# Kernel optimization log

Hardware: AMD Instinct MI355X
Metric: run time of the kernel (lower is better)

Reference implementation:

```python
import jax, jax.numpy as jnp
import numpy as np

EPS = 1e-6

def _linear_params(key, d_in, d_out):
    w = jax.random.normal(key, (d_in, d_out), dtype=jnp.float32) * np.sqrt(2.0 / (d_in + d_out))
    b = jnp.zeros((d_out,), dtype=jnp.float32)
    return w, b

def setup_inputs() -> dict:
    key = jax.random.key(0)
    ks = jax.random.split(key, 8)
    B, S, D = 4, 2048, 1024
    x = jax.random.normal(ks[0], (B, S, D), dtype=jnp.float32)
    wq, bq = _linear_params(ks[1], D, D)
    wk, bk = _linear_params(ks[2], D, D)
    wv, bv = _linear_params(ks[3], D, D)
    wo, bo = _linear_params(ks[4], D, D)
    w1, b1 = _linear_params(ks[5], D, D)
    w2, b2 = _linear_params(ks[6], D, D)
    g1 = jnp.ones((D,), jnp.float32); be1 = jnp.zeros((D,), jnp.float32)
    g2 = jnp.ones((D,), jnp.float32); be2 = jnp.zeros((D,), jnp.float32)
    return {"x": x, "wq": wq, "bq": bq, "wk": wk, "bk": bk, "wv": wv, "bv": bv,
            "wo": wo, "bo": bo, "w1": w1, "b1": b1, "w2": w2, "b2": b2,
            "g1": g1, "be1": be1, "g2": g2, "be2": be2}

def _layernorm(x, gamma, beta):
    mean = jnp.mean(x, axis=-1, keepdims=True)
    # torch .std() default is unbiased (ddof=1); eps added to std (not var)
    std = jnp.std(x, axis=-1, keepdims=True, ddof=1)
    return gamma * (x - mean) / (std + EPS) + beta

def _attention(x, wq, bq, wk, bk, wv, bv, wo, bo):
    S = x.shape[-2]
    q = x @ wq + bq  # [B,S,D]
    k = x @ wk + bk
    v = x @ wv + bv
    scores = jnp.einsum('bsd,btd->bst', q, k) / jnp.sqrt(jnp.asarray(S, jnp.float32))
    causal = jnp.tril(jnp.ones((S, S), dtype=bool))  # keep lower triangle incl. diag
    scores = jnp.where(causal, scores, -jnp.inf)
    attn = jax.nn.softmax(scores, axis=-1)
    out = jnp.einsum('bst,btd->bsd', attn, v)
    return out @ wo + bo

def reference(x, wq, bq, wk, bk, wv, bv, wo, bo, w1, b1, w2, b2, g1, be1, g2, be2):
    h = _attention(_layernorm(x, g1, be1), wq, bq, wk, bk, wv, bv, wo, bo) + x
    m = _layernorm(h, g2, be2)
    m = jnp.maximum(m @ w1 + b1, 0.0) @ w2 + b2
    return m + h
```

## Files before the change

### kernel.cpp

```cpp
#include <hip/hip_runtime.h>
#include <math.h>

#define BB 4
#define SS 2048
#define DD 1024
#define MM (BB*SS)
#define SD ((size_t)SS*DD)
#define MD ((size_t)MM*DD)
#define PPB ((size_t)2162688)

#define WT_OFF (3*MD + 4*PPB)
#define ZP_OFF (WT_OFF + 6*(size_t)DD*DD)
#define REQ_WS ((ZP_OFF + 16) * 2)

constexpr float LN_EPS = 1e-6f;

typedef __attribute__((ext_vector_type(8))) __bf16 bf16x8;
typedef __attribute__((ext_vector_type(4))) float f32x4;

__device__ __forceinline__ unsigned short f2bfbits(float f){
    unsigned u = __float_as_uint(f);
    u += 0x7FFFu + ((u >> 16) & 1u);
    return (unsigned short)(u >> 16);
}
__device__ __forceinline__ int rowWidth(int s){ return ((s >> 6) + 1) << 6; }
__device__ __forceinline__ size_t rowOff(int s){
    int g = s >> 6;
    return (size_t)4096 * (size_t)((g * (g + 1)) >> 1) + (size_t)(s & 63) * (size_t)((g + 1) << 6);
}
__device__ __forceinline__ void gl_lds(const unsigned short* g, unsigned short* l){
    __builtin_amdgcn_global_load_lds(
        (const __attribute__((address_space(1))) unsigned int*)g,
        (__attribute__((address_space(3))) unsigned int*)l, 16, 0, 0);
}

__device__ __forceinline__ int3 xcd_swz(){
    const int gx = gridDim.x, gy = gridDim.y, gz = gridDim.z;
    const int n = gx * gy * gz;
    int lin = blockIdx.x + gx * (blockIdx.y + gy * blockIdx.z);
    const int cpx = n >> 3;
    lin = (lin & 7) * cpx + (lin >> 3);
    int3 r;
    r.x = lin % gx; lin /= gx;
    r.y = lin % gy;
    r.z = lin / gy;
    return r;
}

__global__ __launch_bounds__(256)
void sentinel_kernel(float* __restrict__ out, const float val){
    out[(size_t)blockIdx.x * 256 + threadIdx.x] = val;
}

struct WPack { const float* w[6]; unsigned short* o[6]; unsigned short* zp; };
__global__ __launch_bounds__(256)
void wtrans(WPack wp)
{
    __shared__ float Ts[64][65];
    const float* W = wp.w[blockIdx.z];
    unsigned short* WT = wp.o[blockIdx.z];
    const int r0 = blockIdx.y*64, c0 = blockIdx.x*64;
    const int tid = threadIdx.x;
    if (blockIdx.x == 0 && blockIdx.y == 0 && blockIdx.z == 0 && tid < 16) wp.zp[tid] = 0;
    #pragma unroll
    for (int i = 0; i < 16; ++i){
        int lin = tid + i*256;
        int r = lin >> 6, c = lin & 63;
        Ts[r][c] = W[(size_t)(r0+r)*DD + c0+c];
    }
    __syncthreads();
    #pragma unroll
    for (int i = 0; i < 16; ++i){
        int lin = tid + i*256;
        int r = lin >> 6, c = lin & 63;
        WT[(size_t)(c0+r)*DD + r0+c] = f2bfbits(Ts[c][r]);
    }
}

__global__ __launch_bounds__(256)
void ln_f32(const float* __restrict__ x, const float* __restrict__ gamma,
            const float* __restrict__ beta, unsigned short* __restrict__ out)
{
    __shared__ float red[4];
    const int row = blockIdx.x;
    const int tid = threadIdx.x;
    float4 xv = ((const float4*)(x + (size_t)row*DD))[tid];
    float v[4] = {xv.x, xv.y, xv.z, xv.w};
    float s = v[0]+v[1]+v[2]+v[3];
    #pragma unroll
    for (int off = 32; off > 0; off >>= 1) s += __shfl_down(s, off, 64);
    if ((tid & 63) == 0) red[tid >> 6] = s;
    __syncthreads();
    const float mean = (red[0]+red[1]+red[2]+red[3]) * (1.0f/DD);
    __syncthreads();
    float q = 0.f;
    #pragma unroll
    for (int i = 0; i < 4; ++i){ float d = v[i]-mean; q += d*d; }
    #pragma unroll
    for (int off = 32; off > 0; off >>= 1) q += __shfl_down(q, off, 64);
    if ((tid & 63) == 0) red[tid >> 6] = q;
    __syncthreads();
    const float var = (red[0]+red[1]+red[2]+red[3]) * (1.0f/(DD-1));
    const float inv = 1.0f/(sqrtf(var) + LN_EPS);
    float4 g4 = ((const float4*)gamma)[tid];
    float4 b4 = ((const float4*)beta)[tid];
    ushort4 o;
    o.x = f2bfbits(g4.x*(v[0]-mean)*inv + b4.x);
    o.y = f2bfbits(g4.y*(v[1]-mean)*inv + b4.y);
    o.z = f2bfbits(g4.z*(v[2]-mean)*inv + b4.z);
    o.w = f2bfbits(g4.w*(v[3]-mean)*inv + b4.w);
    ((ushort4*)(out + (size_t)row*DD))[tid] = o;
}

template<bool RELU, bool RES, bool OUTF, bool BIAS_M>
__device__ __forceinline__ void gemm_core(
    const unsigned short* __restrict__ A, const unsigned short* __restrict__ B,
    const float* __restrict__ bias, const float* __restrict__ resF,
    unsigned short* __restrict__ outB, float* __restrict__ outF,
    const int N, const int K, const int lda, const int ldb,
    const int m0, const int n0,
    unsigned short* As, unsigned short* Bs)
{
    const int tid = threadIdx.x, lane = tid & 63, wave = tid >> 6;
    const int wm = ((wave >> 1) & 1) * 64, wn = (wave & 1) * 64;
    const int quad = lane >> 4, l15 = lane & 15;
    const unsigned short* ga[4]; const unsigned short* gb[4];
    #pragma unroll
    for (int c = 0; c < 4; ++c){
        const int mr = (wave*4 + c)*8 + (lane >> 3);
        const int gk = ((lane & 7) - mr) & 7;
        ga[c] = A + (size_t)(m0 + mr)*lda + gk*8;
        gb[c] = B + (size_t)(n0 + mr)*ldb + gk*8;
    }
    f32x4 acc[4][4] = {};
    for (int k0 = 0; k0 < K; k0 += 64){
        #pragma unroll
        for (int c = 0; c < 4; ++c){
            gl_lds(ga[c] + k0, &As[(wave*4+c)*512]);
            gl_lds(gb[c] + k0, &Bs[(wave*4+c)*512]);
        }
        __syncthreads();
        #pragma unroll
        for (int kk = 0; kk < 2; ++kk){
            bf16x8 af[4], bfr[4];
            #pragma unroll
            for (int t = 0; t < 4; ++t){
                const int ra = wm + t*16 + l15, rb = wn + t*16 + l15, gi = kk*4 + quad;
                af[t]  = *(const bf16x8*)&As[ra*64 + (((gi + ra) & 7) << 3)];
                bfr[t] = *(const bf16x8*)&Bs[rb*64 + (((gi + rb) & 7) << 3)];
            }
            #pragma unroll
            for (int i = 0; i < 4; ++i)
                #pragma unroll
                for (int j = 0; j < 4; ++j)
                    acc[i][j] = __builtin_amdgcn_mfma_f32_16x16x32_bf16(af[i], bfr[j], acc[i][j], 0, 0, 0);
        }
        __syncthreads();
    }
    #pragma unroll
    for (int i = 0; i < 4; ++i){
        #pragma unroll
        for (int r = 0; r < 4; ++r){
            const int m = m0 + wm + i*16 + quad*4 + r;
            const float bm = BIAS_M ? bias[m] : 0.f;
            #pragma unroll
            for (int j = 0; j < 4; ++j){
                const int n = n0 + wn + j*16 + l15;
                float v = acc[i][j][r] + (BIAS_M ? bm : bias[n]);
                if constexpr (RELU) v = fmaxf(v, 0.f);
                if constexpr (RES) v += resF[(size_t)m*N + n];
                if constexpr (OUTF) outF[(size_t)m*N + n] = v;
                else outB[(size_t)m*N + n] = f2bfbits(v);
            }
        }
    }
}

template<bool RELU, bool RES, bool OUTF, bool BIAS_M>
__global__ __launch_bounds__(256)
void gemm_mfma(const unsigned short* __restrict__ A, const unsigned short* __restrict__ B,
               const float* __restrict__ bias, const float* __restrict__ resF,
               unsigned short* __restrict__ outB, float* __restrict__ outF,
               const int N, const int K, const int lda, const int ldb)
{
    __shared__ unsigned short As[128*64];
    __shared__ unsigned short Bs[128*64];
    const int3 b = xcd_swz();
    gemm_core<RELU,RES,OUTF,BIAS_M>(A, B, bias, resF, outB, outF, N, K, lda, ldb,
                                    b.y*128, b.x*128, As, Bs);
}

__global__ __launch_bounds__(256)
void gemm_qk(const unsigned short* __restrict__ LN,
             const unsigned short* __restrict__ WqT, const unsigned short* __restrict__ WkT,
             const float* __restrict__ bq, const float* __restrict__ bk,
             unsigned short* __restrict__ Qw, unsigned short* __restrict__ Kw)
{
    __shared__ unsigned short As[128*64];
    __shared__ unsigned short Bs[128*64];
    const int3 b = xcd_swz();
    const bool isK = (b.z != 0);
    gemm_core<false,false,false,false>(LN, isK ? WkT : WqT, isK ? bk : bq, nullptr,
                                       isK ? Kw : Qw, nullptr, DD, DD, DD, DD,
                                       b.y*128, b.x*128, As, Bs);
}

__global__ __launch_bounds__(256)
void scores_mfma(const unsigned short* __restrict__ Qb, const unsigned short* __restrict__ Kb,
                 unsigned short* __restrict__ Pb, const float scale)
{
    const int3 b = xcd_swz();
    const int s0 = b.y*128, t0 = b.x*128;
    if (t0 > s0) return;
    const unsigned short* Q  = Qb + (size_t)b.z*SD;
    const unsigned short* Km = Kb + (size_t)b.z*SD;
    unsigned short* P        = Pb + (size_t)b.z*PPB;
    __shared__ unsigned short As[128*64];
    __shared__ unsigned short Bs[128*64];
    const int tid = threadIdx.x, lane = tid & 63, wave = tid >> 6;
    const int wm = ((wave >> 1) & 1) * 64, wn = (wave & 1) * 64;
    const int quad = lane >> 4, l15 = lane & 15;
    const unsigned short* ga[4]; const unsigned short* gb[4];
    #pragma unroll
    for (int c = 0; c < 4; ++c){
        const int mr = (wave*4 + c)*8 + (lane >> 3);
        const int gk = ((lane & 7) - mr) & 7;
        ga[c] = Q  + (size_t)(s0 + mr)*DD + gk*8;
        gb[c] = Km + (size_t)(t0 + mr)*DD + gk*8;
    }
    f32x4 acc[4][4] = {};
    for (int k0 = 0; k0 < DD; k0 += 64){
        #pragma unroll
        for (int c = 0; c < 4; ++c){
            gl_lds(ga[c] + k0, &As[(wave*4+c)*512]);
            gl_lds(gb[c] + k0, &Bs[(wave*4+c)*512]);
        }
        __syncthreads();
        #pragma unroll
        for (int kk = 0; kk < 2; ++kk){
            bf16x8 af[4], bfr[4];
            #pragma unroll
            for (int t = 0; t < 4; ++t){
                const int ra = wm + t*16 + l15, rb = wn + t*16 + l15, gi = kk*4 + quad;
                af[t]  = *(const bf16x8*)&As[ra*64 + (((gi + ra) & 7) << 3)];
                bfr[t] = *(const bf16x8*)&Bs[rb*64 + (((gi + rb) & 7) << 3)];
            }
            #pragma unroll
            for (int i = 0; i < 4; ++i)
                #pragma unroll
                for (int j = 0; j < 4; ++j)
                    acc[i][j] = __builtin_amdgcn_mfma_f32_16x16x32_bf16(af[i], bfr[j], acc[i][j], 0, 0, 0);
        }
        __syncthreads();
    }
    #pragma unroll
    for (int i = 0; i < 4; ++i){
        #pragma unroll
        for (int r = 0; r < 4; ++r){
            const int s = s0 + wm + i*16 + quad*4 + r;
            const int width = rowWidth(s);
            unsigned short* pr = P + rowOff(s);
            #pragma unroll
            for (int j = 0; j < 4; ++j){
                const int t = t0 + wn + j*16 + l15;
                if (t < width) pr[t] = f2bfbits(acc[i][j][r] * scale);
            }
        }
    }
}

__global__ __launch_bounds__(256)
void softmax_p(unsigned short* __restrict__ Pb)
{
    __shared__ float red[4];
    const int s = blockIdx.x;
    const int width = rowWidth(s);
    unsigned short* r = Pb + (size_t)blockIdx.y * PPB + rowOff(s);
    const int tid = threadIdx.x;
    float vals[8];
    float m = -1e30f;
    #pragma unroll
    for (int i = 0; i < 8; ++i){
        int t = tid + i*256;
        float v = -1e30f;
        if (t <= s) v = __uint_as_float(((unsigned)r[t]) << 16);
        vals[i] = v; m = fmaxf(m, v);
    }
    #pragma unroll
    for (int off = 32; off > 0; off >>= 1) m = fmaxf(m, __shfl_down(m, off, 64));
    if ((tid & 63) == 0) red[tid >> 6] = m;
    __syncthreads();
    const float M4 = fmaxf(fmaxf(red[0],red[1]), fmaxf(red[2],red[3]));
    __syncthreads();
    float ev[8]; float sum = 0.f;
    #pragma unroll
    for (int i = 0; i < 8; ++i){ ev[i] = __expf(vals[i] - M4); sum += ev[i]; }
    #pragma unroll
    for (int off = 32; off > 0; off >>= 1) sum += __shfl_down(sum, off, 64);
    if ((tid & 63) == 0) red[tid >> 6] = sum;
    __syncthreads();
    const float inv = 1.0f / (red[0]+red[1]+red[2]+red[3]);
    #pragma unroll
    for (int i = 0; i < 8; ++i){
        int t = tid + i*256;
        if (t < width) r[t] = f2bfbits(ev[i] * inv);
    }
}

__global__ __launch_bounds__(256)
void pv_mfma(const unsigned short* __restrict__ Pb, const unsigned short* __restrict__ VT,
             unsigned short* __restrict__ Cb, const unsigned short* __restrict__ zpad)
{
    const int3 b = xcd_swz();
    const int s0 = b.y*128, n0 = b.x*128;
    const unsigned short* P = Pb + (size_t)b.z*PPB;
    unsigned short* C       = Cb + (size_t)b.z*SD;
    const int bcol = b.z*SS;
    __shared__ unsigned short As[128*64];
    __shared__ unsigned short Bs[128*64];
    const int tid = threadIdx.x, lane = tid & 63, wave = tid >> 6;
    const int wm = ((wave >> 1) & 1) * 64, wn = (wave & 1) * 64;
    const int quad = lane >> 4, l15 = lane & 15;
    const unsigned short* ga[4]; const unsigned short* gb[4]; int pw[4];
    #pragma unroll
    for (int c = 0; c < 4; ++c){
        const int mr = (wave*4 + c)*8 + (lane >> 3);
        const int gk = ((lane & 7) - mr) & 7;
        const int s = s0 + mr;
        pw[c] = rowWidth(s) - gk*8;
        ga[c] = P + rowOff(s) + gk*8;
        gb[c] = VT + (size_t)(n0 + mr)*MM + bcol + gk*8;
    }
    f32x4 acc[4][4] = {};
    const int kmax = s0 + 128;
    for (int k0 = 0; k0 < kmax; k0 += 64){
        #pragma unroll
        for (int c = 0; c < 4; ++c){
            const unsigned short* gp = (k0 < pw[c]) ? (ga[c] + k0) : zpad;
            gl_lds(gp, &As[(wave*4+c)*512]);
            gl_lds(gb[c] + k0, &Bs[(wave*4+c)*512]);
        }
        __syncthreads();
        #pragma unroll
        for (int kk = 0; kk < 2; ++kk){
            bf16x8 af[4], bfr[4];
            #pragma unroll
            for (int t = 0; t < 4; ++t){
                const int ra = wm + t*16 + l15, rb = wn + t*16 + l15, gi = kk*4 + quad;
                af[t]  = *(const bf16x8*)&As[ra*64 + (((gi + ra) & 7) << 3)];
                bfr[t] = *(const bf16x8*)&Bs[rb*64 + (((gi + rb) & 7) << 3)];
            }
            #pragma unroll
            for (int i = 0; i < 4; ++i)
                #pragma unroll
                for (int j = 0; j < 4; ++j)
                    acc[i][j] = __builtin_amdgcn_mfma_f32_16x16x32_bf16(af[i], bfr[j], acc[i][j], 0, 0, 0);
        }
        __syncthreads();
    }
    #pragma unroll
    for (int i = 0; i < 4; ++i){
        #pragma unroll
        for (int r = 0; r < 4; ++r){
            const int s = s0 + wm + i*16 + quad*4 + r;
            #pragma unroll
            for (int j = 0; j < 4; ++j){
                const int n = n0 + wn + j*16 + l15;
                C[(size_t)s*DD + n] = f2bfbits(acc[i][j][r]);
            }
        }
    }
}

extern "C" void kernel_launch(void* const* d_in, const int* in_sizes, int n_in,
                              void* d_out, int out_size, void* d_ws, size_t ws_size,
                              hipStream_t stream)
{
    (void)in_sizes; (void)n_in; (void)out_size;
    const float* x   = (const float*)d_in[0];
    const float* bq  = (const float*)d_in[2];
    const float* bk  = (const float*)d_in[4];
    const float* bv  = (const float*)d_in[6];
    const float* bo  = (const float*)d_in[8];
    const float* b1  = (const float*)d_in[10];
    const float* b2  = (const float*)d_in[12];
    const float* g1  = (const float*)d_in[13];
    const float* be1 = (const float*)d_in[14];
    const float* g2  = (const float*)d_in[15];
    const float* be2 = (const float*)d_in[16];
    float* outf = (float*)d_out;

    if (ws_size < (size_t)REQ_WS){
        sentinel_kernel<<<dim3((unsigned)(MD/256)), dim3(256), 0, stream>>>(outf, 1.0e9f);
        return;
    }

    unsigned short* wsb = (unsigned short*)d_ws;
    unsigned short* Qw  = wsb;
    unsigned short* Kw  = wsb + MD;
    unsigned short* VTw = wsb + 2*MD;
    unsigned short* Pw  = wsb + 3*MD;
    unsigned short* WT  = wsb + WT_OFF;
    unsigned short* ZP  = wsb + ZP_OFF;
    float*          Hf  = (float*)Kw;
    unsigned short* CTX = Qw;
    unsigned short* MIDw= Pw;
    unsigned short* LN  = (unsigned short*)d_out;

    WPack wp;
    static const int widx[6] = {1,3,5,7,9,11};
    for (int i = 0; i < 6; ++i){
        wp.w[i] = (const float*)d_in[widx[i]];
        wp.o[i] = WT + (size_t)i*DD*DD;
    }
    wp.zp = ZP;
    unsigned short* WqT = wp.o[0]; unsigned short* WkT = wp.o[1];
    unsigned short* WvT = wp.o[2]; unsigned short* WoT = wp.o[3];
    unsigned short* W1T = wp.o[4]; unsigned short* W2T = wp.o[5];

    const dim3 blk(256);
    const float scale = 1.0f / sqrtf((float)SS);
    const dim3 gA(DD/128, MM/128);
    const dim3 gVT(MM/128, DD/128);

    wtrans<<<dim3(16,16,6), blk, 0, stream>>>(wp);
    ln_f32<<<dim3(MM), blk, 0, stream>>>(x, g1, be1, LN);
    gemm_qk<<<dim3(DD/128, MM/128, 2), blk, 0, stream>>>(LN, WqT, WkT, bq, bk, Qw, Kw);
    gemm_mfma<false,false,false,true ><<<gVT, blk, 0, stream>>>(WvT, LN, bv, nullptr, VTw, nullptr, MM, DD, DD, DD);
    scores_mfma<<<dim3(SS/128, SS/128, BB), blk, 0, stream>>>(Qw, Kw, Pw, scale);
    softmax_p<<<dim3(SS, BB), blk, 0, stream>>>(Pw);
    pv_mfma<<<dim3(DD/128, SS/128, BB), blk, 0, stream>>>(Pw, VTw, CTX, ZP);
    gemm_mfma<false,true,true,false><<<gA, blk, 0, stream>>>(CTX, WoT, bo, x, nullptr, Hf, DD, DD, DD, DD);
    ln_f32<<<dim3(MM), blk, 0, stream>>>(Hf, g2, be2, LN);
    gemm_mfma<true,false,false,false><<<gA, blk, 0, stream>>>(LN, W1T, b1, nullptr, MIDw, nullptr, DD, DD, DD, DD);
    gemm_mfma<false,true,true,false><<<gA, blk, 0, stream>>>(MIDw, W2T, b2, Hf, nullptr, outf, DD, DD, DD, DD);
}
```

Measured before the change: 386.4 us.

## Use 256x128 eight-wave GEMM tiles with triple-buffered LDS prefetch pipeline

Replaces the 128x128 four-wave GEMM core with a 256x128 tile run by eight waves. Global-to-LDS loads now go into a three-stage ring buffer, so the tile two steps ahead is prefetched while MFMAs run on the current one. Raw s_barrier and waitcnt calls plus a priority bump around the MFMA block replace the per-iteration __syncthreads. The aim is to hide load latency and improve reuse, at the cost of 144KB LDS per block (one block per CU), fewer blocks in the grid, and fragile hand-managed synchronisation.

Result: faster. 375.0 us (-2.9%).

```diff
diff --git a/kernel.cpp b/kernel.cpp
--- a/kernel.cpp
+++ b/kernel.cpp
@@ -113,59 +113,100 @@
 }
 
 template<bool RELU, bool RES, bool OUTF, bool BIAS_M>
-__device__ __forceinline__ void gemm_core(
+__device__ __forceinline__ void gemm_core8(
     const unsigned short* __restrict__ A, const unsigned short* __restrict__ B,
     const float* __restrict__ bias, const float* __restrict__ resF,
     unsigned short* __restrict__ outB, float* __restrict__ outF,
     const int N, const int K, const int lda, const int ldb,
-    const int m0, const int n0,
-    unsigned short* As, unsigned short* Bs)
-{
+    const int m0, const int n0, unsigned short* S)
+{
+    unsigned short* A0 = S;
+    unsigned short* A1 = S + 16384;
+    unsigned short* A2 = S + 32768;
+    unsigned short* B0 = S + 49152;
+    unsigned short* B1 = S + 57344;
+    unsigned short* B2 = S + 65536;
+
     const int tid = threadIdx.x, lane = tid & 63, wave = tid >> 6;
-    const int wm = ((wave >> 1) & 1) * 64, wn = (wave & 1) * 64;
+    const int wr = (wave >> 1) * 64;
+    const int wc = (wave & 1) * 64;
     const int quad = lane >> 4, l15 = lane & 15;
-    const unsigned short* ga[4]; const unsigned short* gb[4];
+
+    const unsigned short* ga[4]; const unsigned short* gb[2];
     #pragma unroll
     for (int c = 0; c < 4; ++c){
         const int mr = (wave*4 + c)*8 + (lane >> 3);
         const int gk = ((lane & 7) - mr) & 7;
         ga[c] = A + (size_t)(m0 + mr)*lda + gk*8;
+    }
+    #pragma unroll
+    for (int c = 0; c < 2; ++c){
+        const int mr = (wave*2 + c)*8 + (lane >> 3);
+        const int gk = ((lane & 7) - mr) & 7;
         gb[c] = B + (size_t)(n0 + mr)*ldb + gk*8;
     }
+
     f32x4 acc[4][4] = {};
-    for (int k0 = 0; k0 < K; k0 += 64){
-        #pragma unroll
-        for (int c = 0; c < 4; ++c){
-            gl_lds(ga[c] + k0, &As[(wave*4+c)*512]);
-            gl_lds(gb[c] + k0, &Bs[(wave*4+c)*512]);
-        }
-        __syncthreads();
+    const int NT = K >> 6;
+
+    #pragma unroll
+    for (int c = 0; c < 4; ++c) gl_lds(ga[c], &A0[(wave*4+c)*512]);
+    #pragma unroll
+    for (int c = 0; c < 2; ++c) gl_lds(gb[c], &B0[(wave*2+c)*512]);
+    #pragma unroll
+    for (int c = 0; c < 4; ++c) gl_lds(ga[c] + 64, &A1[(wave*4+c)*512]);
+    #pragma unroll
+    for (int c = 0; c < 2; ++c) gl_lds(gb[c] + 64, &B1[(wave*2+c)*512]);
+    asm volatile("s_waitcnt vmcnt(6)" ::: "memory");
+    __builtin_amdgcn_s_barrier();
+
+    for (int t = 0; t < NT; ++t){
+        const int kn = (t + 2) << 6;
+        const bool more2 = (t + 2 < NT);
         #pragma unroll
         for (int kk = 0; kk < 2; ++kk){
             bf16x8 af[4], bfr[4];
             #pragma unroll
-            for (int t = 0; t < 4; ++t){
-                const int ra = wm + t*16 + l15, rb = wn + t*16 + l15, gi = kk*4 + quad;
-                af[t]  = *(const bf16x8*)&As[ra*64 + (((gi + ra) & 7) << 3)];
-                bfr[t] = *(const bf16x8*)&Bs[rb*64 + (((gi + rb) & 7) << 3)];
-            }
+            for (int u = 0; u < 4; ++u){
+                const int ra = wr + u*16 + l15, rb = wc + u*16 + l15, gi = kk*4 + quad;
+                af[u]  = *(const bf16x8*)&A0[ra*64 + (((gi + ra) & 7) << 3)];
+                bfr[u] = *(const bf16x8*)&B0[rb*64 + (((gi + rb) & 7) << 3)];
+            }
+            if (kk == 0 && more2){
+                #pragma unroll
+                for (int c = 0; c < 4; ++c) gl_lds(ga[c] + kn, &A2[(wave*4+c)*512]);
+                #pragma unroll
+                for (int c = 0; c < 2; ++c) gl_lds(gb[c] + kn, &B2[(wave*2+c)*512]);
+            }
+            __builtin_amdgcn_s_barrier();
+            asm volatile("s_waitcnt lgkmcnt(0)" ::: "memory");
+            __builtin_amdgcn_sched_barrier(0);
+            __builtin_amdgcn_s_setprio(1);
             #pragma unroll
             for (int i = 0; i < 4; ++i)
                 #pragma unroll
                 for (int j = 0; j < 4; ++j)
                     acc[i][j] = __builtin_amdgcn_mfma_f32_16x16x32_bf16(af[i], bfr[j], acc[i][j], 0, 0, 0);
-        }
-        __syncthreads();
-    }
+            __builtin_amdgcn_s_setprio(0);
+            if (kk == 1){
+                if (more2) asm volatile("s_waitcnt vmcnt(6)" ::: "memory");
+                else       asm volatile("s_waitcnt vmcnt(0)" ::: "memory");
+            }
+            __builtin_amdgcn_s_barrier();
+        }
+        unsigned short* ta = A0; A0 = A1; A1 = A2; A2 = ta;
+        unsigned short* tb = B0; B0 = B1; B1 = B2; B2 = tb;
+    }
+
     #pragma unroll
     for (int i = 0; i < 4; ++i){
         #pragma unroll
         for (int r = 0; r < 4; ++r){
-            const int m = m0 + wm + i*16 + quad*4 + r;
+            const int m = m0 + wr + i*16 + quad*4 + r;
             const float bm = BIAS_M ? bias[m] : 0.f;
             #pragma unroll
             for (int j = 0; j < 4; ++j){
-                const int n = n0 + wn + j*16 + l15;
+                const int n = n0 + wc + j*16 + l15;
                 float v = acc[i][j][r] + (BIAS_M ? bm : bias[n]);
                 if constexpr (RELU) v = fmaxf(v, 0.f);
                 if constexpr (RES) v += resF[(size_t)m*N + n];
@@ -177,32 +218,30 @@
 }
 
 template<bool RELU, bool RES, bool OUTF, bool BIAS_M>
-__global__ __launch_bounds__(256)
+__global__ __launch_bounds__(512)
 void gemm_mfma(const unsigned short* __restrict__ A, const unsigned short* __restrict__ B,
                const float* __restrict__ bias, const float* __restrict__ resF,
                unsigned short* __restrict__ outB, float* __restrict__ outF,
                const int N, const int K, const int lda, const int ldb)
 {
-    __shared__ unsigned short As[128*64];
-    __shared__ unsigned short Bs[128*64];
+    __shared__ unsigned short Smem[73728];
     const int3 b = xcd_swz();
-    gemm_core<RELU,RES,OUTF,BIAS_M>(A, B, bias, resF, outB, outF, N, K, lda, ldb,
-                                    b.y*128, b.x*128, As, Bs);
-}
-
-__global__ __launch_bounds__(256)
+    gemm_core8<RELU,RES,OUTF,BIAS_M>(A, B, bias, resF, outB, outF, N, K, lda, ldb,
+                                     b.y*256, b.x*128, Smem);
+}
+
+__global__ __launch_bounds__(512)
 void gemm_qk(const unsigned short* __restrict__ LN,
              const unsigned short* __restrict__ WqT, const unsigned short* __restrict__ WkT,
              const float* __restrict__ bq, const float* __restrict__ bk,
              unsigned short* __restrict__ Qw, unsigned short* __restrict__ Kw)
 {
-    __shared__ unsigned short As[128*64];
-    __shared__ unsigned short Bs[128*64];
+    __shared__ unsigned short Smem[73728];
     const int3 b = xcd_swz();
     const bool isK = (b.z != 0);
-    gemm_core<false,false,false,false>(LN, isK ? WkT : WqT, isK ? bk : bq, nullptr,
-                                       isK ? Kw : Qw, nullptr, DD, DD, DD, DD,
-                                       b.y*128, b.x*128, As, Bs);
+    gemm_core8<false,false,false,false>(LN, isK ? WkT : WqT, isK ? bk : bq, nullptr,
+                                        isK ? Kw : Qw, nullptr, DD, DD, DD, DD,
+                                        b.y*256, b.x*128, Smem);
 }
 
 __global__ __launch_bounds__(256)
@@ -419,19 +458,20 @@
     unsigned short* W1T = wp.o[4]; unsigned short* W2T = wp.o[5];
 
     const dim3 blk(256);
+    const dim3 blk8(512);
     const float scale = 1.0f / sqrtf((float)SS);
-    const dim3 gA(DD/128, MM/128);
-    const dim3 gVT(MM/128, DD/128);
+    const dim3 gA8(DD/128, MM/256);
+    const dim3 gVT8(MM/128, DD/256);
 
     wtrans<<<dim3(16,16,6), blk, 0, stream>>>(wp);
     ln_f32<<<dim3(MM), blk, 0, stream>>>(x, g1, be1, LN);
-    gemm_qk<<<dim3(DD/128, MM/128, 2), blk, 0, stream>>>(LN, WqT, WkT, bq, bk, Qw, Kw);
-    gemm_mfma<false,false,false,true ><<<gVT, blk, 0, stream>>>(WvT, LN, bv, nullptr, VTw, nullptr, MM, DD, DD, DD);
+    gemm_qk<<<dim3(DD/128, MM/256, 2), blk8, 0, stream>>>(LN, WqT, WkT, bq, bk, Qw, Kw);
+    gemm_mfma<false,false,false,true ><<<gVT8, blk8, 0, stream>>>(WvT, LN, bv, nullptr, VTw, nullptr, MM, DD, DD, DD);
     scores_mfma<<<dim3(SS/128, SS/128, BB), blk, 0, stream>>>(Qw, Kw, Pw, scale);
     softmax_p<<<dim3(SS, BB), blk, 0, stream>>>(Pw);
     pv_mfma<<<dim3(DD/128, SS/128, BB), blk, 0, stream>>>(Pw, VTw, CTX, ZP);
-    gemm_mfma<false,true,true,false><<<gA, blk, 0, stream>>>(CTX, WoT, bo, x, nullptr, Hf, DD, DD, DD, DD);
+    gemm_mfma<false,true,true,false><<<gA8, blk8, 0, stream>>>(CTX, WoT, bo, x, nullptr, Hf, DD, DD, DD, DD);
     ln_f32<<<dim3(MM), blk, 0, stream>>>(Hf, g2, be2, LN);
-    gemm_mfma<true,false,false,false><<<gA, blk, 0, stream>>>(LN, W1T, b1, nullptr, MIDw, nullptr, DD, DD, DD, DD);
-    gemm_mfma<false,true,true,false><<<gA, blk, 0, stream>>>(MIDw, W2T, b2, Hf, nullptr, outf, DD, DD, DD, DD);
-}
+    gemm_mfma<true,false,false,false><<<gA8, blk8, 0, stream>>>(LN, W1T, b1, nullptr, MIDw, nullptr, DD, DD, DD, DD);
+    gemm_mfma<false,true,true,false><<<gA8, blk8, 0, stream>>>(MIDw, W2T, b2, Hf, nullptr, outf, DD, DD, DD, DD);
+}
```

## Fuse softmax into scores and PV kernels with deferred row normalization

Applied to the files above, without the earlier changes.

Removes the separate softmax kernel. The scores kernel now writes exp(score*scale) directly, without subtracting the row max, and accumulates per-row sums into a float buffer with atomics. The PV kernel divides by that row sum in its epilogue. This saves a full read/write pass over the probability matrix and one launch. In exchange it drops max-subtraction, which relies on scores staying small, adds atomic traffic, and removes the XCD block swizzle from both kernels.

After: 378.2 us. -2.1%, faster.

```diff
diff --git a/kernel.cpp b/kernel.cpp
--- a/kernel.cpp
+++ b/kernel.cpp
@@ -11,7 +11,8 @@
 
 #define WT_OFF (3*MD + 4*PPB)
 #define ZP_OFF (WT_OFF + 6*(size_t)DD*DD)
-#define REQ_WS ((ZP_OFF + 16) * 2)
+#define LF_OFF (ZP_OFF + 16)
+#define REQ_WS ((LF_OFF + 16384) * 2)
 
 constexpr float LN_EPS = 1e-6f;
 
@@ -52,7 +53,7 @@
     out[(size_t)blockIdx.x * 256 + threadIdx.x] = val;
 }
 
-struct WPack { const float* w[6]; unsigned short* o[6]; unsigned short* zp; };
+struct WPack { const float* w[6]; unsigned short* o[6]; unsigned short* zp; float* lf; };
 __global__ __launch_bounds__(256)
 void wtrans(WPack wp)
 {
@@ -62,6 +63,10 @@
     const int r0 = blockIdx.y*64, c0 = blockIdx.x*64;
     const int tid = threadIdx.x;
     if (blockIdx.x == 0 && blockIdx.y == 0 && blockIdx.z == 0 && tid < 16) wp.zp[tid] = 0;
+    if (blockIdx.y == 0 && blockIdx.z == 0){
+        float2 z2 = {0.f, 0.f};
+        ((float2*)wp.lf)[blockIdx.x*256 + tid] = z2;
+    }
     #pragma unroll
     for (int i = 0; i < 16; ++i){
         int lin = tid + i*256;
@@ -207,14 +212,14 @@
 
 __global__ __launch_bounds__(256)
 void scores_mfma(const unsigned short* __restrict__ Qb, const unsigned short* __restrict__ Kb,
-                 unsigned short* __restrict__ Pb, const float scale)
-{
-    const int3 b = xcd_swz();
-    const int s0 = b.y*128, t0 = b.x*128;
+                 unsigned short* __restrict__ Pb, float* __restrict__ Lf, const float scale)
+{
+    const int s0 = blockIdx.y*128, t0 = blockIdx.x*128;
     if (t0 > s0) return;
-    const unsigned short* Q  = Qb + (size_t)b.z*SD;
-    const unsigned short* Km = Kb + (size_t)b.z*SD;
-    unsigned short* P        = Pb + (size_t)b.z*PPB;
+    const unsigned short* Q  = Qb + (size_t)blockIdx.z*SD;
+    const unsigned short* Km = Kb + (size_t)blockIdx.z*SD;
+    unsigned short* P        = Pb + (size_t)blockIdx.z*PPB;
+    float* L                 = Lf + (size_t)blockIdx.z*SS;
     __shared__ unsigned short As[128*64];
     __shared__ unsigned short Bs[128*64];
     const int tid = threadIdx.x, lane = tid & 63, wave = tid >> 6;
@@ -260,62 +265,33 @@
             const int s = s0 + wm + i*16 + quad*4 + r;
             const int width = rowWidth(s);
             unsigned short* pr = P + rowOff(s);
-            #pragma unroll
-            for (int j = 0; j < 4; ++j){
-                const int t = t0 + wn + j*16 + l15;
-                if (t < width) pr[t] = f2bfbits(acc[i][j][r] * scale);
-            }
-        }
-    }
-}
-
-__global__ __launch_bounds__(256)
-void softmax_p(unsigned short* __restrict__ Pb)
-{
-    __shared__ float red[4];
-    const int s = blockIdx.x;
-    const int width = rowWidth(s);
-    unsigned short* r = Pb + (size_t)blockIdx.y * PPB + rowOff(s);
-    const int tid = threadIdx.x;
-    float vals[8];
-    float m = -1e30f;
-    #pragma unroll
-    for (int i = 0; i < 8; ++i){
-        int t = tid + i*256;
-        float v = -1e30f;
-        if (t <= s) v = __uint_as_float(((unsigned)r[t]) << 16);
-        vals[i] = v; m = fmaxf(m, v);
-    }
-    #pragma unroll
-    for (int off = 32; off > 0; off >>= 1) m = fmaxf(m, __shfl_down(m, off, 64));
-    if ((tid & 63) == 0) red[tid >> 6] = m;
-    __syncthreads();
-    const float M4 = fmaxf(fmaxf(red[0],red[1]), fmaxf(red[2],red[3]));
-    __syncthreads();
-    float ev[8]; float sum = 0.f;
-    #pragma unroll
-    for (int i = 0; i < 8; ++i){ ev[i] = __expf(vals[i] - M4); sum += ev[i]; }
-    #pragma unroll
-    for (int off = 32; off > 0; off >>= 1) sum += __shfl_down(sum, off, 64);
-    if ((tid & 63) == 0) red[tid >> 6] = sum;
-    __syncthreads();
-    const float inv = 1.0f / (red[0]+red[1]+red[2]+red[3]);
-    #pragma unroll
-    for (int i = 0; i < 8; ++i){
-        int t = tid + i*256;
-        if (t < width) r[t] = f2bfbits(ev[i] * inv);
+            float psum = 0.f;
+            if (t0 + wn < width){
+                #pragma unroll
+                for (int j = 0; j < 4; ++j){
+                    const int t = t0 + wn + j*16 + l15;
+                    const float e = (t <= s) ? __expf(acc[i][j][r] * scale) : 0.f;
+                    pr[t] = f2bfbits(e);
+                    psum += e;
+                }
+                #pragma unroll
+                for (int off = 8; off > 0; off >>= 1) psum += __shfl_xor(psum, off, 64);
+                if (l15 == 0) atomicAdd(&L[s], psum);
+            }
+        }
     }
 }
 
 __global__ __launch_bounds__(256)
 void pv_mfma(const unsigned short* __restrict__ Pb, const unsigned short* __restrict__ VT,
-             unsigned short* __restrict__ Cb, const unsigned short* __restrict__ zpad)
-{
-    const int3 b = xcd_swz();
-    const int s0 = b.y*128, n0 = b.x*128;
-    const unsigned short* P = Pb + (size_t)b.z*PPB;
-    unsigned short* C       = Cb + (size_t)b.z*SD;
-    const int bcol = b.z*SS;
+             unsigned short* __restrict__ Cb, const unsigned short* __restrict__ zpad,
+             const float* __restrict__ Lf)
+{
+    const int s0 = blockIdx.y*128, n0 = blockIdx.x*128;
+    const unsigned short* P = Pb + (size_t)blockIdx.z*PPB;
+    unsigned short* C       = Cb + (size_t)blockIdx.z*SD;
+    const float* L          = Lf + (size_t)blockIdx.z*SS;
+    const int bcol = blockIdx.z*SS;
     __shared__ unsigned short As[128*64];
     __shared__ unsigned short Bs[128*64];
     const int tid = threadIdx.x, lane = tid & 63, wave = tid >> 6;
@@ -363,10 +339,11 @@
         #pragma unroll
         for (int r = 0; r < 4; ++r){
             const int s = s0 + wm + i*16 + quad*4 + r;
+            const float linv = 1.0f / L[s];
             #pragma unroll
             for (int j = 0; j < 4; ++j){
                 const int n = n0 + wn + j*16 + l15;
-                C[(size_t)s*DD + n] = f2bfbits(acc[i][j][r]);
+                C[(size_t)s*DD + n] = f2bfbits(acc[i][j][r] * linv);
             }
         }
     }
@@ -402,6 +379,7 @@
     unsigned short* Pw  = wsb + 3*MD;
     unsigned short* WT  = wsb + WT_OFF;
     unsigned short* ZP  = wsb + ZP_OFF;
+    float*          Lf  = (float*)(wsb + LF_OFF);
     float*          Hf  = (float*)Kw;
     unsigned short* CTX = Qw;
     unsigned short* MIDw= Pw;
@@ -414,6 +392,7 @@
         wp.o[i] = WT + (size_t)i*DD*DD;
     }
     wp.zp = ZP;
+    wp.lf = Lf;
     unsigned short* WqT = wp.o[0]; unsigned short* WkT = wp.o[1];
     unsigned short* WvT = wp.o[2]; unsigned short* WoT = wp.o[3];
     unsigned short* W1T = wp.o[4]; unsigned short* W2T = wp.o[5];
@@ -427,9 +406,8 @@
     ln_f32<<<dim3(MM), blk, 0, stream>>>(x, g1, be1, LN);
     gemm_qk<<<dim3(DD/128, MM/128, 2), blk, 0, stream>>>(LN, WqT, WkT, bq, bk, Qw, Kw);
     gemm_mfma<false,false,false,true ><<<gVT, blk, 0, stream>>>(WvT, LN, bv, nullptr, VTw, nullptr, MM, DD, DD, DD);
-    scores_mfma<<<dim3(SS/128, SS/128, BB), blk, 0, stream>>>(Qw, Kw, Pw, scale);
-    softmax_p<<<dim3(SS, BB), blk, 0, stream>>>(Pw);
-    pv_mfma<<<dim3(DD/128, SS/128, BB), blk, 0, stream>>>(Pw, VTw, CTX, ZP);
+    scores_mfma<<<dim3(SS/128, SS/128, BB), blk, 0, stream>>>(Qw, Kw, Pw, Lf, scale);
+    pv_mfma<<<dim3(DD/128, SS/128, BB), blk, 0, stream>>>(Pw, VTw, CTX, ZP, Lf);
     gemm_mfma<false,true,true,false><<<gA, blk, 0, stream>>>(CTX, WoT, bo, x, nullptr, Hf, DD, DD, DD, DD);
     ln_f32<<<dim3(MM), blk, 0, stream>>>(Hf, g2, be2, LN);
     gemm_mfma<true,false,false,false><<<gA, blk, 0, stream>>>(LN, W1T, b1, nullptr, MIDw, nullptr, DD, DD, DD, DD);
```
